# Kernel optimization log

Hardware: AMD Instinct MI355X
Metric: run time of the kernel (lower is better)

## Reference

```python
import jax, jax.numpy as jnp
import numpy as np

B, S, D = 2, 2048, 2048
H = 16
NOPE, ROPE, DV = 128, 64, 128
DQK = NOPE + ROPE  # 192
QLR, KVLR = 1536, 512


def setup_inputs() -> dict:
    key = jax.random.key(0)
    ks = jax.random.split(key, 8)
    hidden_states = jax.random.normal(ks[0], (B, S, D), dtype=jnp.float32) * 0.02
    sequence_mask = jnp.ones((B, S), dtype=bool)
    # rotary frequencies (complex exponential split into cos/sin), theta=10000
    inv_freq = 1.0 / (10000.0 ** (np.arange(0, ROPE, 2, dtype=np.float32) / ROPE))
    angles = np.outer(np.arange(S, dtype=np.float32), inv_freq)  # [S, ROPE//2]
    freqs_cos = jnp.asarray(np.cos(angles), dtype=jnp.float32)
    freqs_sin = jnp.asarray(np.sin(angles), dtype=jnp.float32)
    def lin(k, fan_in, fan_out):
        return jax.random.normal(k, (fan_in, fan_out), dtype=jnp.float32) / np.sqrt(fan_in)
    return {
        'hidden_states': hidden_states,
        'sequence_mask': sequence_mask,
        'freqs_cos': freqs_cos,
        'freqs_sin': freqs_sin,
        'Wq_down': lin(ks[1], D, QLR),
        'Wkv_down': lin(ks[2], D, KVLR + ROPE),
        'Wq_up': lin(ks[3], QLR, H * DQK),
        'Wkv_up': lin(ks[4], KVLR, H * (DV + NOPE)),
        'Wo': lin(ks[5], H * DV, D),
    }


def _rmsnorm(x, eps=1e-5):
    return x * jax.lax.rsqrt(jnp.mean(x * x, axis=-1, keepdims=True) + eps)


def _apply_rope(x, cos, sin):
    # x: [B,S,H,d] with interleaved (real, imag) pairs; cos/sin: [S, d//2]
    b, s, h, d = x.shape
    xr = x.reshape(b, s, h, d // 2, 2)
    x0, x1 = xr[..., 0], xr[..., 1]
    c = cos[None, :s, None, :]
    sn = sin[None, :s, None, :]
    y = jnp.stack([x0 * c - x1 * sn, x0 * sn + x1 * c], axis=-1)
    return y.reshape(b, s, h, d)


def reference(hidden_states, sequence_mask, freqs_cos, freqs_sin,
              Wq_down, Wkv_down, Wq_up, Wkv_up, Wo):
    b, s, _ = hidden_states.shape
    # Q path: down-project -> rmsnorm -> up-project
    q_latent = _rmsnorm(hidden_states @ Wq_down)
    q = (q_latent @ Wq_up).reshape(b, s, H, DQK)
    q_nope, q_rope = q[..., :NOPE], q[..., NOPE:]
    q_rope = _apply_rope(q_rope, freqs_cos, freqs_sin)
    q = jnp.concatenate([q_rope, q_nope], axis=-1)  # [B,S,H,DQK]
    # KV path
    kvdr = hidden_states @ Wkv_down  # [B,S,KVLR+ROPE]
    kv_latent, k_rope = kvdr[..., :KVLR], kvdr[..., KVLR:]
    k_rope = _apply_rope(k_rope.reshape(b, s, 1, ROPE), freqs_cos, freqs_sin)
    k_rope = jnp.broadcast_to(k_rope, (b, s, H, ROPE))
    kv = _rmsnorm(kv_latent) @ Wkv_up  # [B,S,H*(NOPE+DV)]
    k_nope = kv[..., :H * NOPE].reshape(b, s, H, NOPE)
    v = kv[..., H * NOPE:].reshape(b, s, H, DV)
    k = jnp.concatenate([k_rope, k_nope], axis=-1)  # [B,S,H,DQK]
    # causal attention (flash_attn_varlen with full masks == per-batch causal)
    scale = 1.0 / np.sqrt(DQK)
    scores = jnp.einsum('bqhd,bkhd->bhqk', q, k) * scale
    causal = jnp.tril(jnp.ones((s, s), dtype=bool))
    mask = causal[None, None, :, :] & sequence_mask[:, None, None, :]
    scores = jnp.where(mask, scores, jnp.float32(-1e9))
    attn = jax.nn.softmax(scores, axis=-1)
    out = jnp.einsum('bhqk,bkhd->bqhd', attn, v).reshape(b, s, H * DV)
    return out @ Wo
```

## Files before the change

kernel.cpp:

```cpp
#include <hip/hip_runtime.h>
#include <math.h>


typedef unsigned short u16;
typedef __attribute__((ext_vector_type(8))) __bf16 bf16x8;
typedef __attribute__((ext_vector_type(4))) float f32x4;

#define DEV static __device__ __forceinline__

DEV float b2f(u16 v) { return __uint_as_float(((unsigned int)v) << 16); }
DEV u16 f2b(float f) {
  unsigned int u = __float_as_uint(f);
  u += 0x7fffu + ((u >> 16) & 1u);
  return (u16)(u >> 16);
}

DEV float waveReduceSum(float v) {
  #pragma unroll
  for (int o = 32; o > 0; o >>= 1) v += __shfl_down(v, o, 64);
  return v;
}

DEV void gld16(const u16* g, u16* l) {
  __builtin_amdgcn_global_load_lds((const __attribute__((address_space(1))) void*)g,
                                   (__attribute__((address_space(3))) void*)l, 16, 0, 0);
}

__global__ __launch_bounds__(256)
void cvt_f32_bf16(const float* __restrict__ in, u16* __restrict__ out, int n4) {
  int i = blockIdx.x * 256 + threadIdx.x;
  if (i < n4) {
    float4 v = reinterpret_cast<const float4*>(in)[i];
    ushort4 o;
    o.x = f2b(v.x); o.y = f2b(v.y); o.z = f2b(v.z); o.w = f2b(v.w);
    reinterpret_cast<ushort4*>(out)[i] = o;
  }
}

__global__ __launch_bounds__(256)
void transpose_f32_bf16(const float* __restrict__ in, u16* __restrict__ out, int R, int C) {
  __shared__ u16 tile[32][33];
  int c0 = blockIdx.x * 32, r0 = blockIdx.y * 32;
  for (int i = threadIdx.y; i < 32; i += 8)
    tile[i][threadIdx.x] = f2b(in[(size_t)(r0 + i) * C + c0 + threadIdx.x]);
  __syncthreads();
  for (int i = threadIdx.y; i < 32; i += 8)
    out[(size_t)(c0 + i) * R + r0 + threadIdx.x] = tile[threadIdx.x][i];
}

template<int OUT_BF16>
__global__ __launch_bounds__(256)
void gemm_bt(const u16* __restrict__ A, const u16* __restrict__ BT, void* __restrict__ Cp,
             int M, int N, int K) {
  __shared__ __attribute__((aligned(16))) u16 As[4096];
  __shared__ __attribute__((aligned(16))) u16 Bs[4096];
  const int tid = threadIdx.x;
  const int lane = tid & 63;
  const int wave = tid >> 6;
  const int wm = (wave >> 1) * 64;
  const int wn = (wave & 1) * 64;
  const int q = lane >> 4;
  const int l16 = lane & 15;

  const int gx = gridDim.x;
  const int nwg = gx * gridDim.y;
  const int orig = blockIdx.y * gx + blockIdx.x;
  const int cpx = nwg >> 3;
  const int swz = (orig & 7) * cpx + (orig >> 3);
  const int bm = (swz / gx) * 128;
  const int bn = (swz % gx) * 128;

  f32x4 zero = {0.f, 0.f, 0.f, 0.f};
  f32x4 acc[4][4];
  #pragma unroll
  for (int i = 0; i < 4; i++)
    #pragma unroll
    for (int j = 0; j < 4; j++) acc[i][j] = zero;

  for (int k0 = 0; k0 < K; k0 += 32) {
    #pragma unroll
    for (int i = 0; i < 2; i++) {
      int jb = i * 256 + wave * 64;
      int u = jb + lane;
      int row = u >> 2;
      int kq = (u & 3) ^ ((u >> 3) & 3);
      gld16(A + (size_t)(bm + row) * K + k0 + kq * 8, As + jb * 8);
      int rB = bn + row;
      if (rB >= N) rB = N - 1;
      gld16(BT + (size_t)rB * K + k0 + kq * 8, Bs + jb * 8);
    }
    __syncthreads();
    bf16x8 af[4], bfr[4];
    #pragma unroll
    for (int t = 0; t < 4; t++) {
      int rowA = wm + t * 16 + l16;
      int rowB = wn + t * 16 + l16;
      int uA = (rowA << 2) | (q ^ ((rowA >> 1) & 3));
      int uB = (rowB << 2) | (q ^ ((rowB >> 1) & 3));
      af[t]  = *reinterpret_cast<const bf16x8*>(As + uA * 8);
      bfr[t] = *reinterpret_cast<const bf16x8*>(Bs + uB * 8);
    }
    #pragma unroll
    for (int mt = 0; mt < 4; mt++)
      #pragma unroll
      for (int nt = 0; nt < 4; nt++)
        acc[mt][nt] = __builtin_amdgcn_mfma_f32_16x16x32_bf16(af[mt], bfr[nt], acc[mt][nt], 0, 0, 0);
    __syncthreads();
  }

  float* Cf = (float*)Cp;
  u16* Cb = (u16*)Cp;
  #pragma unroll
  for (int mt = 0; mt < 4; mt++) {
    #pragma unroll
    for (int nt = 0; nt < 4; nt++) {
      int col = bn + wn + nt * 16 + l16;
      if (col < N) {
        int row0 = bm + wm + mt * 16 + q * 4;
        #pragma unroll
        for (int r = 0; r < 4; r++) {
          size_t idx = (size_t)(row0 + r) * N + col;
          float v = acc[mt][nt][r];
          if (OUT_BF16) Cb[idx] = f2b(v); else Cf[idx] = v;
        }
      }
    }
  }
}

__global__ __launch_bounds__(256)
void rmsnorm_rows(const float* __restrict__ in, u16* __restrict__ out, int C, int stride) {
  int row = blockIdx.x;
  const float* x = in + (size_t)row * stride;
  float ss = 0.f;
  for (int i = threadIdx.x; i < C; i += 256) { float v = x[i]; ss += v * v; }
  ss = waveReduceSum(ss);
  __shared__ float red[4];
  __shared__ float s_scale;
  int lane = threadIdx.x & 63, wid = threadIdx.x >> 6;
  if (lane == 0) red[wid] = ss;
  __syncthreads();
  if (threadIdx.x == 0)
    s_scale = rsqrtf((red[0] + red[1] + red[2] + red[3]) / (float)C + 1e-5f);
  __syncthreads();
  float sc = s_scale;
  u16* o = out + (size_t)row * C;
  for (int i = threadIdx.x; i < C; i += 256) o[i] = f2b(x[i] * sc);
}

__global__ __launch_bounds__(256)
void rope_pack_q(const u16* __restrict__ q2, const float* __restrict__ fc, const float* __restrict__ fs,
                 u16* __restrict__ Q) {
  const float scale = 0.07216878364870323f;
  int bs = blockIdx.x;
  int b = bs >> 11, s = bs & 2047;
  __shared__ float c[32], sn[32];
  if (threadIdx.x < 32) {
    c[threadIdx.x] = fc[s * 32 + threadIdx.x];
    sn[threadIdx.x] = fs[s * 32 + threadIdx.x];
  }
  __syncthreads();
  const u16* qrow = q2 + (size_t)bs * 3072;
  for (int t = threadIdx.x; t < 512; t += 256) {
    int h = t >> 5, i = t & 31;
    float x0 = b2f(qrow[h * 192 + 128 + 2 * i]);
    float x1 = b2f(qrow[h * 192 + 128 + 2 * i + 1]);
    size_t base = ((size_t)(b * 16 + h) * 2048 + s) * 192;
    Q[base + 2 * i]     = f2b((x0 * c[i] - x1 * sn[i]) * scale);
    Q[base + 2 * i + 1] = f2b((x0 * sn[i] + x1 * c[i]) * scale);
  }
  for (int t = threadIdx.x; t < 2048; t += 256) {
    int h = t >> 7, j = t & 127;
    Q[((size_t)(b * 16 + h) * 2048 + s) * 192 + 64 + j] = f2b(b2f(qrow[h * 192 + j]) * scale);
  }
}

__global__ __launch_bounds__(256)
void kv_split(const float* __restrict__ t13, const float* __restrict__ fc, const float* __restrict__ fs,
              u16* __restrict__ kvl, u16* __restrict__ krope) {
  int row = blockIdx.x;
  int s = row & 2047;
  const float* x = t13 + (size_t)row * 2112 + 1536;
  float ss = 0.f;
  for (int i = threadIdx.x; i < 512; i += 256) { float v = x[i]; ss += v * v; }
  ss = waveReduceSum(ss);
  __shared__ float red[4];
  __shared__ float s_scale;
  int lane = threadIdx.x & 63, wid = threadIdx.x >> 6;
  if (lane == 0) red[wid] = ss;
  __syncthreads();
  if (threadIdx.x == 0)
    s_scale = rsqrtf((red[0] + red[1] + red[2] + red[3]) * (1.0f / 512.0f) + 1e-5f);
  __syncthreads();
  float sc = s_scale;
  for (int i = threadIdx.x; i < 512; i += 256) kvl[(size_t)row * 512 + i] = f2b(x[i] * sc);
  if (threadIdx.x < 32) {
    int i = threadIdx.x;
    float cc = fc[s * 32 + i], sn = fs[s * 32 + i];
    float x0 = x[512 + 2 * i], x1 = x[512 + 2 * i + 1];
    krope[(size_t)row * 64 + 2 * i]     = f2b(x0 * cc - x1 * sn);
    krope[(size_t)row * 64 + 2 * i + 1] = f2b(x0 * sn + x1 * cc);
  }
}

__global__ __launch_bounds__(256)
void assemble_kv2(const u16* __restrict__ kvb, const u16* __restrict__ krope,
                  u16* __restrict__ Kc, u16* __restrict__ Vt) {
  int ks = blockIdx.x;
  int bh = blockIdx.y;
  int b = bh >> 4, h = bh & 15;
  int t = threadIdx.x;
  if (t < 192) {
    int kq = t >> 3, sl = t & 7;
    int s = ks * 8 + sl;
    size_t bs = (size_t)(b * 2048 + s);
    uint4 v;
    if (kq < 8) v = *reinterpret_cast<const uint4*>(krope + bs * 64 + kq * 8);
    else        v = *reinterpret_cast<const uint4*>(kvb + bs * 4096 + h * 128 + (kq - 8) * 8);
    *reinterpret_cast<uint4*>(Kc + (((size_t)bh * 24 + kq) * 2048 + s) * 8) = v;
  }
  if (t < 128) {
    int dv = t;
    u16 tmp[8];
    #pragma unroll
    for (int j = 0; j < 8; j++) {
      int s = ks * 8 + j;
      tmp[j] = kvb[(size_t)(b * 2048 + s) * 4096 + 2048 + h * 128 + dv];
    }
    *reinterpret_cast<uint4*>(Vt + (((size_t)bh * 256 + ks) * 128 + dv) * 8) = *reinterpret_cast<uint4*>(tmp);
  }
}

__global__ __launch_bounds__(256, 2)
void flash_attn5(const u16* __restrict__ Q, const u16* __restrict__ Kc,
                 const u16* __restrict__ Vt, u16* __restrict__ O) {
  __shared__ __attribute__((aligned(16))) u16 Ks[24 * 64 * 8];
  __shared__ __attribute__((aligned(16))) u16 Vs[8 * 128 * 8];
  __shared__ __attribute__((aligned(16))) u16 Ps[4 * 16 * 72];

  const int blk = blockIdx.x;
  const int bh = ((blk & 7) << 2) | (blk >> 7);
  const int tpair = (blk >> 3) & 15;
  const int b = bh >> 4, h = bh & 15;
  const int tid = threadIdx.x, lane = tid & 63, wave = tid >> 6;
  const int quad = lane >> 4, l16 = lane & 15;
  u16* PsW = Ps + wave * 16 * 72;

  bf16x8 onesf;
  #pragma unroll
  for (int j = 0; j < 8; j++) onesf[j] = (l16 == 0) ? (__bf16)1.0f : (__bf16)0.0f;

  for (int phase = 0; phase < 2; phase++) {
    const int qt = phase == 0 ? tpair : 31 - tpair;
    const int q0 = qt * 64;
    const int nk = (qt + 1) * 64;

    bf16x8 qf[6];
    {
      int qrow = q0 + wave * 16 + l16;
      const u16* qp = Q + ((size_t)bh * 2048 + qrow) * 192 + quad * 8;
      #pragma unroll
      for (int kc = 0; kc < 6; kc++)
        qf[kc] = *reinterpret_cast<const bf16x8*>(qp + kc * 32);
    }

    f32x4 zero = {0.f, 0.f, 0.f, 0.f};
    f32x4 oacc[9];
    #pragma unroll
    for (int nt = 0; nt < 9; nt++) oacc[nt] = zero;

    for (int k0 = 0; k0 < nk; k0 += 64) {
      __syncthreads();
      #pragma unroll
      for (int ii = 0; ii < 6; ii++) {
        int kq = wave * 6 + ii;
        gld16(Kc + (((size_t)bh * 24 + kq) * 2048 + k0 + lane) * 8, Ks + kq * 64 * 8);
      }
      #pragma unroll
      for (int jj = 0; jj < 4; jj++) {
        int vc = wave * 4 + jj;
        int kc = vc >> 1, dvh = vc & 1;
        gld16(Vt + (((size_t)bh * 256 + (k0 >> 3) + kc) * 128 + dvh * 64 + lane) * 8,
              Vs + (kc * 128 + dvh * 64) * 8);
      }
      __syncthreads();

      f32x4 sacc[4];
      #pragma unroll
      for (int nt = 0; nt < 4; nt++) sacc[nt] = zero;
      #pragma unroll
      for (int kc = 0; kc < 6; kc++) {
        #pragma unroll
        for (int nt = 0; nt < 4; nt++) {
          bf16x8 kb = *reinterpret_cast<const bf16x8*>(Ks + ((kc * 4 + quad) * 64 + nt * 16 + l16) * 8);
          sacc[nt] = __builtin_amdgcn_mfma_f32_16x16x32_bf16(qf[kc], kb, sacc[nt], 0, 0, 0);
        }
      }

      #pragma unroll
      for (int r = 0; r < 4; r++) {
        int qrow_g = q0 + wave * 16 + quad * 4 + r;
        #pragma unroll
        for (int nt = 0; nt < 4; nt++) {
          int key = k0 + nt * 16 + l16;
          float p = (key <= qrow_g) ? __expf(sacc[nt][r]) : 0.f;
          PsW[(quad * 4 + r) * 72 + nt * 16 + l16] = f2b(p);
        }
      }

      #pragma unroll
      for (int kcp = 0; kcp < 2; kcp++) {
        bf16x8 pa = *reinterpret_cast<const bf16x8*>(PsW + l16 * 72 + kcp * 32 + quad * 8);
        #pragma unroll
        for (int nt = 0; nt < 8; nt++) {
          bf16x8 vb = *reinterpret_cast<const bf16x8*>(Vs + ((kcp * 4 + quad) * 128 + nt * 16 + l16) * 8);
          oacc[nt] = __builtin_amdgcn_mfma_f32_16x16x32_bf16(pa, vb, oacc[nt], 0, 0, 0);
        }
        oacc[8] = __builtin_amdgcn_mfma_f32_16x16x32_bf16(pa, onesf, oacc[8], 0, 0, 0);
      }
    }

    #pragma unroll
    for (int r = 0; r < 4; r++) {
      float l = __shfl(oacc[8][r], lane & 48, 64);
      float inv = 1.0f / l;
      int s = q0 + wave * 16 + quad * 4 + r;
      #pragma unroll
      for (int nt = 0; nt < 8; nt++)
        O[((size_t)b * 2048 + s) * 2048 + h * 128 + nt * 16 + l16] = f2b(oacc[nt][r] * inv);
    }
  }
}

extern "C" void kernel_launch(void* const* d_in, const int* in_sizes, int n_in,
                              void* d_out, int out_size, void* d_ws, size_t ws_size,
                              hipStream_t stream) {
  (void)in_sizes; (void)n_in; (void)out_size; (void)ws_size;
  const float* hs   = (const float*)d_in[0];
  const float* fc   = (const float*)d_in[2];
  const float* fs   = (const float*)d_in[3];
  const float* Wqd  = (const float*)d_in[4];
  const float* Wkvd = (const float*)d_in[5];
  const float* Wqu  = (const float*)d_in[6];
  const float* Wkvu = (const float*)d_in[7];
  const float* Wo   = (const float*)d_in[8];

  char* ws = (char*)d_ws;
  size_t off = 0;
  auto alloc = [&](size_t bytes) { size_t o = off; off += (bytes + 255) & ~(size_t)255; return o; };
  const size_t oHS   = alloc(16777216);
  const size_t oRA   = alloc(16777216);
  const size_t oRB   = alloc(25165824);
  const size_t oRC   = alloc(12582912);
  const size_t oRD   = alloc(25165824);
  const size_t oRE   = alloc(34603008);
  const size_t oKVL  = alloc(4194304);
  const size_t oKR   = alloc(524288);
  const size_t oW13T  = alloc(8650752);
  const size_t oWquT  = alloc(9437184);
  const size_t oWkvuT = alloc(4194304);
  const size_t oWoT   = alloc(8388608);

  u16* hs_bf = (u16*)(ws + oHS);
  u16* Vt   = (u16*)(ws + oRA);
  u16* q2   = (u16*)(ws + oRB);
  u16* Kc   = (u16*)(ws + oRB);
  u16* qlat = (u16*)(ws + oRC);
  u16* Qb   = (u16*)(ws + oRD);
  float* t13 = (float*)(ws + oRE);
  u16* kvb  = (u16*)(ws + oRE);
  u16* attn_out = (u16*)(ws + oRE);
  u16* kvl  = (u16*)(ws + oKVL);
  u16* krope = (u16*)(ws + oKR);
  u16* W13T  = (u16*)(ws + oW13T);
  u16* WquT  = (u16*)(ws + oWquT);
  u16* WkvuT = (u16*)(ws + oWkvuT);
  u16* WoT   = (u16*)(ws + oWoT);

  cvt_f32_bf16<<<8192, 256, 0, stream>>>(hs, hs_bf, 2097152);
  dim3 tb(32, 8);
  transpose_f32_bf16<<<dim3(48, 64), tb, 0, stream>>>(Wqd, W13T, 2048, 1536);
  transpose_f32_bf16<<<dim3(18, 64), tb, 0, stream>>>(Wkvd, W13T + (size_t)1536 * 2048, 2048, 576);
  transpose_f32_bf16<<<dim3(96, 48), tb, 0, stream>>>(Wqu, WquT, 1536, 3072);
  transpose_f32_bf16<<<dim3(128, 16), tb, 0, stream>>>(Wkvu, WkvuT, 512, 4096);
  transpose_f32_bf16<<<dim3(64, 64), tb, 0, stream>>>(Wo, WoT, 2048, 2048);

  gemm_bt<0><<<dim3(17, 32), 256, 0, stream>>>(hs_bf, W13T, t13, 4096, 2112, 2048);
  rmsnorm_rows<<<4096, 256, 0, stream>>>(t13, qlat, 1536, 2112);
  gemm_bt<1><<<dim3(24, 32), 256, 0, stream>>>(qlat, WquT, q2, 4096, 3072, 1536);
  rope_pack_q<<<4096, 256, 0, stream>>>(q2, fc, fs, Qb);
  kv_split<<<4096, 256, 0, stream>>>(t13, fc, fs, kvl, krope);
  gemm_bt<1><<<dim3(32, 32), 256, 0, stream>>>(kvl, WkvuT, kvb, 4096, 4096, 512);
  assemble_kv2<<<dim3(256, 32), 256, 0, stream>>>(kvb, krope, Kc, Vt);
  flash_attn5<<<dim3(512), 256, 0, stream>>>(Qb, Kc, Vt, attn_out);
  gemm_bt<0><<<dim3(16, 32), 256, 0, stream>>>(attn_out, WoT, (float*)d_out, 4096, 2048, 2048);
}
```

Before: 470.2 us.

## Double-buffer K/V tiles and process 128-row query tiles per attention block

The attention kernel now gives each wave two 16-row query subtiles, so a block covers 128 query rows and reuses each staged K/V tile twice as much. K/V loads go into double-buffered shared memory, and the next tile's async loads are issued before computing the current one, with explicit vmcnt waits. The grid is halved to 256 blocks with launch bounds of 1 block per CU. This cuts global traffic per FLOP and hides load latency, but costs register and LDS pressure and fewer blocks for occupancy and load balance.

Result: slower. 501.3 us (+6.6%).

```diff
diff --git a/kernel.cpp b/kernel.cpp
--- a/kernel.cpp
+++ b/kernel.cpp
@@ -231,103 +231,134 @@
   }
 }
 
-__global__ __launch_bounds__(256, 2)
-void flash_attn5(const u16* __restrict__ Q, const u16* __restrict__ Kc,
+__global__ __launch_bounds__(256, 1)
+void flash_attn6(const u16* __restrict__ Q, const u16* __restrict__ Kc,
                  const u16* __restrict__ Vt, u16* __restrict__ O) {
-  __shared__ __attribute__((aligned(16))) u16 Ks[24 * 64 * 8];
-  __shared__ __attribute__((aligned(16))) u16 Vs[8 * 128 * 8];
-  __shared__ __attribute__((aligned(16))) u16 Ps[4 * 16 * 72];
+  __shared__ __attribute__((aligned(16))) u16 Ks[2][24 * 64 * 8];
+  __shared__ __attribute__((aligned(16))) u16 Vs[2][8 * 128 * 8];
+  __shared__ __attribute__((aligned(16))) u16 Ps[4 * 32 * 72];
 
   const int blk = blockIdx.x;
-  const int bh = ((blk & 7) << 2) | (blk >> 7);
-  const int tpair = (blk >> 3) & 15;
+  const int xcd = blk & 7;
+  const int i = blk >> 3;
+  const int tpair = i & 7;
+  const int bh = (xcd << 2) | (i >> 3);
   const int b = bh >> 4, h = bh & 15;
   const int tid = threadIdx.x, lane = tid & 63, wave = tid >> 6;
   const int quad = lane >> 4, l16 = lane & 15;
-  u16* PsW = Ps + wave * 16 * 72;
+  u16* PsW = Ps + wave * 32 * 72;
 
   bf16x8 onesf;
   #pragma unroll
   for (int j = 0; j < 8; j++) onesf[j] = (l16 == 0) ? (__bf16)1.0f : (__bf16)0.0f;
 
+  auto stage = [&](u16* KsB, u16* VsB, int kk) {
+    #pragma unroll
+    for (int ii = 0; ii < 6; ii++) {
+      int kq = wave * 6 + ii;
+      gld16(Kc + (((size_t)bh * 24 + kq) * 2048 + kk + lane) * 8, KsB + kq * 64 * 8);
+    }
+    #pragma unroll
+    for (int jj = 0; jj < 4; jj++) {
+      int vc = wave * 4 + jj, kc = vc >> 1, dvh = vc & 1;
+      gld16(Vt + (((size_t)bh * 256 + (kk >> 3) + kc) * 128 + dvh * 64 + lane) * 8,
+            VsB + (kc * 128 + dvh * 64) * 8);
+    }
+  };
+
   for (int phase = 0; phase < 2; phase++) {
-    const int qt = phase == 0 ? tpair : 31 - tpair;
-    const int q0 = qt * 64;
-    const int nk = (qt + 1) * 64;
-
-    bf16x8 qf[6];
-    {
-      int qrow = q0 + wave * 16 + l16;
+    const int qt = phase == 0 ? tpair : 15 - tpair;
+    const int q0 = qt * 128;
+    const int nk = (qt + 1) * 128;
+
+    bf16x8 qf[2][6];
+    #pragma unroll
+    for (int mt = 0; mt < 2; mt++) {
+      int qrow = q0 + wave * 32 + mt * 16 + l16;
       const u16* qp = Q + ((size_t)bh * 2048 + qrow) * 192 + quad * 8;
       #pragma unroll
       for (int kc = 0; kc < 6; kc++)
-        qf[kc] = *reinterpret_cast<const bf16x8*>(qp + kc * 32);
+        qf[mt][kc] = *reinterpret_cast<const bf16x8*>(qp + kc * 32);
     }
 
     f32x4 zero = {0.f, 0.f, 0.f, 0.f};
-    f32x4 oacc[9];
-    #pragma unroll
-    for (int nt = 0; nt < 9; nt++) oacc[nt] = zero;
+    f32x4 oacc[2][9];
+    #pragma unroll
+    for (int mt = 0; mt < 2; mt++)
+      #pragma unroll
+      for (int nt = 0; nt < 9; nt++) oacc[mt][nt] = zero;
 
     for (int k0 = 0; k0 < nk; k0 += 64) {
-      __syncthreads();
-      #pragma unroll
-      for (int ii = 0; ii < 6; ii++) {
-        int kq = wave * 6 + ii;
-        gld16(Kc + (((size_t)bh * 24 + kq) * 2048 + k0 + lane) * 8, Ks + kq * 64 * 8);
-      }
-      #pragma unroll
-      for (int jj = 0; jj < 4; jj++) {
-        int vc = wave * 4 + jj;
-        int kc = vc >> 1, dvh = vc & 1;
-        gld16(Vt + (((size_t)bh * 256 + (k0 >> 3) + kc) * 128 + dvh * 64 + lane) * 8,
-              Vs + (kc * 128 + dvh * 64) * 8);
-      }
-      __syncthreads();
-
-      f32x4 sacc[4];
-      #pragma unroll
-      for (int nt = 0; nt < 4; nt++) sacc[nt] = zero;
+      const int cur = (k0 >> 6) & 1;
+      __builtin_amdgcn_s_barrier();
+      if (k0 == 0) stage(Ks[0], Vs[0], 0);
+      if (k0 + 64 < nk) {
+        stage(Ks[cur ^ 1], Vs[cur ^ 1], k0 + 64);
+        asm volatile("s_waitcnt vmcnt(10)" ::: "memory");
+      } else {
+        asm volatile("s_waitcnt vmcnt(0)" ::: "memory");
+      }
+      __builtin_amdgcn_sched_barrier(0);
+      __builtin_amdgcn_s_barrier();
+
+      const u16* KsC = Ks[cur];
+      const u16* VsC = Vs[cur];
+
+      f32x4 sacc[2][4];
+      #pragma unroll
+      for (int mt = 0; mt < 2; mt++)
+        #pragma unroll
+        for (int nt = 0; nt < 4; nt++) sacc[mt][nt] = zero;
       #pragma unroll
       for (int kc = 0; kc < 6; kc++) {
         #pragma unroll
         for (int nt = 0; nt < 4; nt++) {
-          bf16x8 kb = *reinterpret_cast<const bf16x8*>(Ks + ((kc * 4 + quad) * 64 + nt * 16 + l16) * 8);
-          sacc[nt] = __builtin_amdgcn_mfma_f32_16x16x32_bf16(qf[kc], kb, sacc[nt], 0, 0, 0);
+          bf16x8 kb = *reinterpret_cast<const bf16x8*>(KsC + ((kc * 4 + quad) * 64 + nt * 16 + l16) * 8);
+          sacc[0][nt] = __builtin_amdgcn_mfma_f32_16x16x32_bf16(qf[0][kc], kb, sacc[0][nt], 0, 0, 0);
+          sacc[1][nt] = __builtin_amdgcn_mfma_f32_16x16x32_bf16(qf[1][kc], kb, sacc[1][nt], 0, 0, 0);
         }
       }
 
       #pragma unroll
+      for (int mt = 0; mt < 2; mt++) {
+        #pragma unroll
+        for (int r = 0; r < 4; r++) {
+          int qrow_g = q0 + wave * 32 + mt * 16 + quad * 4 + r;
+          #pragma unroll
+          for (int nt = 0; nt < 4; nt++) {
+            int key = k0 + nt * 16 + l16;
+            float p = (key <= qrow_g) ? __expf(sacc[mt][nt][r]) : 0.f;
+            PsW[(mt * 16 + quad * 4 + r) * 72 + nt * 16 + l16] = f2b(p);
+          }
+        }
+      }
+
+      #pragma unroll
+      for (int kcp = 0; kcp < 2; kcp++) {
+        bf16x8 pa0 = *reinterpret_cast<const bf16x8*>(PsW + (l16) * 72 + kcp * 32 + quad * 8);
+        bf16x8 pa1 = *reinterpret_cast<const bf16x8*>(PsW + (16 + l16) * 72 + kcp * 32 + quad * 8);
+        #pragma unroll
+        for (int nt = 0; nt < 8; nt++) {
+          bf16x8 vb = *reinterpret_cast<const bf16x8*>(VsC + ((kcp * 4 + quad) * 128 + nt * 16 + l16) * 8);
+          oacc[0][nt] = __builtin_amdgcn_mfma_f32_16x16x32_bf16(pa0, vb, oacc[0][nt], 0, 0, 0);
+          oacc[1][nt] = __builtin_amdgcn_mfma_f32_16x16x32_bf16(pa1, vb, oacc[1][nt], 0, 0, 0);
+        }
+        oacc[0][8] = __builtin_amdgcn_mfma_f32_16x16x32_bf16(pa0, onesf, oacc[0][8], 0, 0, 0);
+        oacc[1][8] = __builtin_amdgcn_mfma_f32_16x16x32_bf16(pa1, onesf, oacc[1][8], 0, 0, 0);
+      }
+    }
+
+    #pragma unroll
+    for (int mt = 0; mt < 2; mt++) {
+      #pragma unroll
       for (int r = 0; r < 4; r++) {
-        int qrow_g = q0 + wave * 16 + quad * 4 + r;
-        #pragma unroll
-        for (int nt = 0; nt < 4; nt++) {
-          int key = k0 + nt * 16 + l16;
-          float p = (key <= qrow_g) ? __expf(sacc[nt][r]) : 0.f;
-          PsW[(quad * 4 + r) * 72 + nt * 16 + l16] = f2b(p);
-        }
-      }
-
-      #pragma unroll
-      for (int kcp = 0; kcp < 2; kcp++) {
-        bf16x8 pa = *reinterpret_cast<const bf16x8*>(PsW + l16 * 72 + kcp * 32 + quad * 8);
-        #pragma unroll
-        for (int nt = 0; nt < 8; nt++) {
-          bf16x8 vb = *reinterpret_cast<const bf16x8*>(Vs + ((kcp * 4 + quad) * 128 + nt * 16 + l16) * 8);
-          oacc[nt] = __builtin_amdgcn_mfma_f32_16x16x32_bf16(pa, vb, oacc[nt], 0, 0, 0);
-        }
-        oacc[8] = __builtin_amdgcn_mfma_f32_16x16x32_bf16(pa, onesf, oacc[8], 0, 0, 0);
-      }
-    }
-
-    #pragma unroll
-    for (int r = 0; r < 4; r++) {
-      float l = __shfl(oacc[8][r], lane & 48, 64);
-      float inv = 1.0f / l;
-      int s = q0 + wave * 16 + quad * 4 + r;
-      #pragma unroll
-      for (int nt = 0; nt < 8; nt++)
-        O[((size_t)b * 2048 + s) * 2048 + h * 128 + nt * 16 + l16] = f2b(oacc[nt][r] * inv);
+        float l = __shfl(oacc[mt][8][r], lane & 48, 64);
+        float inv = 1.0f / l;
+        int s = q0 + wave * 32 + mt * 16 + quad * 4 + r;
+        #pragma unroll
+        for (int nt = 0; nt < 8; nt++)
+          O[((size_t)b * 2048 + s) * 2048 + h * 128 + nt * 16 + l16] = f2b(oacc[mt][nt][r] * inv);
+      }
     }
   }
 }
@@ -392,6 +423,6 @@
   kv_split<<<4096, 256, 0, stream>>>(t13, fc, fs, kvl, krope);
   gemm_bt<1><<<dim3(32, 32), 256, 0, stream>>>(kvl, WkvuT, kvb, 4096, 4096, 512);
   assemble_kv2<<<dim3(256, 32), 256, 0, stream>>>(kvb, krope, Kc, Vt);
-  flash_attn5<<<dim3(512), 256, 0, stream>>>(Qb, Kc, Vt, attn_out);
+  flash_attn6<<<dim3(256), 256, 0, stream>>>(Qb, Kc, Vt, attn_out);
   gemm_bt<0><<<dim3(16, 32), 256, 0, stream>>>(attn_out, WoT, (float*)d_out, 4096, 2048, 2048);
 }
```

## Double-buffer K tiles and overlap V load with QK compute in flash attention

Applied to the files above, without the earlier changes.

Prefetches the next K tile into a second LDS buffer while the current tile is computed. The V tile load is issued at the start of each iteration but is only waited on after the score/exp stage, using explicit vmcnt waits and raw s_barrier. This is meant to hide global-to-LDS load latency behind the MFMA work, at the cost of extra LDS and one more barrier per iteration.

Result: no change. 470.7 us (+0.1%).

```diff
diff --git a/kernel.cpp b/kernel.cpp
--- a/kernel.cpp
+++ b/kernel.cpp
@@ -232,9 +232,9 @@
 }
 
 __global__ __launch_bounds__(256, 2)
-void flash_attn5(const u16* __restrict__ Q, const u16* __restrict__ Kc,
+void flash_attn7(const u16* __restrict__ Q, const u16* __restrict__ Kc,
                  const u16* __restrict__ Vt, u16* __restrict__ O) {
-  __shared__ __attribute__((aligned(16))) u16 Ks[24 * 64 * 8];
+  __shared__ __attribute__((aligned(16))) u16 Ks[2][24 * 64 * 8];
   __shared__ __attribute__((aligned(16))) u16 Vs[8 * 128 * 8];
   __shared__ __attribute__((aligned(16))) u16 Ps[4 * 16 * 72];
 
@@ -250,6 +250,22 @@
   #pragma unroll
   for (int j = 0; j < 8; j++) onesf[j] = (l16 == 0) ? (__bf16)1.0f : (__bf16)0.0f;
 
+  auto stageK = [&](u16* KsB, int kk) {
+    #pragma unroll
+    for (int ii = 0; ii < 6; ii++) {
+      int kq = wave * 6 + ii;
+      gld16(Kc + (((size_t)bh * 24 + kq) * 2048 + kk + lane) * 8, KsB + kq * 64 * 8);
+    }
+  };
+  auto stageV = [&](int kk) {
+    #pragma unroll
+    for (int jj = 0; jj < 4; jj++) {
+      int vc = wave * 4 + jj, kc = vc >> 1, dvh = vc & 1;
+      gld16(Vt + (((size_t)bh * 256 + (kk >> 3) + kc) * 128 + dvh * 64 + lane) * 8,
+            Vs + (kc * 128 + dvh * 64) * 8);
+    }
+  };
+
   for (int phase = 0; phase < 2; phase++) {
     const int qt = phase == 0 ? tpair : 31 - tpair;
     const int q0 = qt * 64;
@@ -270,20 +286,24 @@
     for (int nt = 0; nt < 9; nt++) oacc[nt] = zero;
 
     for (int k0 = 0; k0 < nk; k0 += 64) {
-      __syncthreads();
-      #pragma unroll
-      for (int ii = 0; ii < 6; ii++) {
-        int kq = wave * 6 + ii;
-        gld16(Kc + (((size_t)bh * 24 + kq) * 2048 + k0 + lane) * 8, Ks + kq * 64 * 8);
+      const int cur = (k0 >> 6) & 1;
+      const bool hasnext = (k0 + 64 < nk);
+
+      __builtin_amdgcn_s_barrier();
+      __builtin_amdgcn_sched_barrier(0);
+      if (k0 == 0) stageK(Ks[0], 0);
+      stageV(k0);
+      if (hasnext) {
+        stageK(Ks[cur ^ 1], k0 + 64);
+        asm volatile("s_waitcnt vmcnt(10)" ::: "memory");
+      } else {
+        asm volatile("s_waitcnt vmcnt(4)" ::: "memory");
       }
-      #pragma unroll
-      for (int jj = 0; jj < 4; jj++) {
-        int vc = wave * 4 + jj;
-        int kc = vc >> 1, dvh = vc & 1;
-        gld16(Vt + (((size_t)bh * 256 + (k0 >> 3) + kc) * 128 + dvh * 64 + lane) * 8,
-              Vs + (kc * 128 + dvh * 64) * 8);
-      }
-      __syncthreads();
+      __builtin_amdgcn_sched_barrier(0);
+      __builtin_amdgcn_s_barrier();
+      __builtin_amdgcn_sched_barrier(0);
+
+      const u16* KsC = Ks[cur];
 
       f32x4 sacc[4];
       #pragma unroll
@@ -292,7 +312,7 @@
       for (int kc = 0; kc < 6; kc++) {
         #pragma unroll
         for (int nt = 0; nt < 4; nt++) {
-          bf16x8 kb = *reinterpret_cast<const bf16x8*>(Ks + ((kc * 4 + quad) * 64 + nt * 16 + l16) * 8);
+          bf16x8 kb = *reinterpret_cast<const bf16x8*>(KsC + ((kc * 4 + quad) * 64 + nt * 16 + l16) * 8);
           sacc[nt] = __builtin_amdgcn_mfma_f32_16x16x32_bf16(qf[kc], kb, sacc[nt], 0, 0, 0);
         }
       }
@@ -307,6 +327,12 @@
           PsW[(quad * 4 + r) * 72 + nt * 16 + l16] = f2b(p);
         }
       }
+
+      if (hasnext) asm volatile("s_waitcnt vmcnt(6)" ::: "memory");
+      else         asm volatile("s_waitcnt vmcnt(0)" ::: "memory");
+      __builtin_amdgcn_sched_barrier(0);
+      __builtin_amdgcn_s_barrier();
+      __builtin_amdgcn_sched_barrier(0);
 
       #pragma unroll
       for (int kcp = 0; kcp < 2; kcp++) {
@@ -392,6 +418,6 @@
   kv_split<<<4096, 256, 0, stream>>>(t13, fc, fs, kvl, krope);
   gemm_bt<1><<<dim3(32, 32), 256, 0, stream>>>(kvl, WkvuT, kvb, 4096, 4096, 512);
   assemble_kv2<<<dim3(256, 32), 256, 0, stream>>>(kvb, krope, Kc, Vt);
-  flash_attn5<<<dim3(512), 256, 0, stream>>>(Qb, Kc, Vt, attn_out);
+  flash_attn7<<<dim3(512), 256, 0, stream>>>(Qb, Kc, Vt, attn_out);
   gemm_bt<0><<<dim3(16, 32), 256, 0, stream>>>(attn_out, WoT, (float*)d_out, 4096, 2048, 2048);
 }
```
